# Optimization experiments

Hardware: AMD Instinct MI355X
Metric: run time of the kernel (lower is better)

The kernel has to match this reference:

```python
import jax, jax.numpy as jnp
import numpy as np

D_MODEL = 1024
HEADS = 16


def setup_inputs() -> dict:
    key = jax.random.key(0)
    ks = jax.random.split(key, 11)
    B, S, D = 2, 2048, D_MODEL
    scale = 1.0 / np.sqrt(D)
    inp = {
        "q": jax.random.normal(ks[0], (B, S, D), jnp.float32),
        "k": jax.random.normal(ks[1], (B, S, D), jnp.float32),
        "v": jax.random.normal(ks[2], (B, S, D), jnp.float32),
        "w_q": jax.random.normal(ks[3], (D, D), jnp.float32) * scale,
        "b_q": jnp.zeros((D,), jnp.float32),
        "w_k": jax.random.normal(ks[4], (D, D), jnp.float32) * scale,
        "b_k": jnp.zeros((D,), jnp.float32),
        "w_v": jax.random.normal(ks[5], (D, D), jnp.float32) * scale,
        "b_v": jnp.zeros((D,), jnp.float32),
        "w_o": jax.random.normal(ks[6], (D, D), jnp.float32) * scale,
        "b_o": jnp.zeros((D,), jnp.float32),
    }
    return inp


def reference(q, k, v, w_q, b_q, w_k, b_k, w_v, b_v, w_o, b_o):
    B, S, D = q.shape
    H = HEADS
    Dh = D // H

    def split(x):  # [B,S,D] -> [B,H,S,Dh]
        return x.reshape(B, S, H, Dh).transpose(0, 2, 1, 3)

    qh = split(q @ w_q + b_q)
    kh = split(k @ w_k + b_k)
    vh = split(v @ w_v + b_v)

    # scaled dot-product attention: softmax(Q K^T / sqrt(Dh)) V
    scores = jnp.einsum("bhsd,bhtd->bhst", qh, kh) / jnp.sqrt(
        jnp.asarray(Dh, qh.dtype)
    )
    attn = jax.nn.softmax(scores, axis=-1)
    out = jnp.einsum("bhst,bhtd->bhsd", attn, vh)

    concat = out.transpose(0, 2, 1, 3).reshape(B, S, D)
    return concat @ w_o + b_o
```

## Files before the change

kernel.cpp:

```cpp
#include <hip/hip_runtime.h>
#include <hip/hip_bf16.h>
#include <math.h>

using bf16 = __hip_bfloat16;
typedef __bf16 bf16x8v __attribute__((ext_vector_type(8)));
typedef float f32x4v __attribute__((ext_vector_type(4)));

#define AS1 __attribute__((address_space(1)))
#define AS3 __attribute__((address_space(3)))

__device__ __forceinline__ void g2l16(const void* g, void* l) {
  __builtin_amdgcn_global_load_lds((const AS1 void*)g, (AS3 void*)l, 16, 0, 0);
}

__device__ __forceinline__ float fclamp(float v) {
  return fminf(fmaxf(v, -6.0e4f), 6.0e4f);
}

#define QSCL 0.1803368801111204f

__global__ __launch_bounds__(256) void transpose_cvt4(
    const float* __restrict__ w0, const float* __restrict__ w1,
    const float* __restrict__ w2, const float* __restrict__ w3,
    bf16* __restrict__ o0, bf16* __restrict__ o1,
    bf16* __restrict__ o2, bf16* __restrict__ o3) {
  const float* in = (blockIdx.z == 0) ? w0 : (blockIdx.z == 1) ? w1
                    : (blockIdx.z == 2) ? w2 : w3;
  bf16* out = (blockIdx.z == 0) ? o0 : (blockIdx.z == 1) ? o1
              : (blockIdx.z == 2) ? o2 : o3;
  __shared__ alignas(16) bf16 tile[64][80];
  const int t = threadIdx.x;
  const int bx = blockIdx.x * 64, by = blockIdx.y * 64;
#pragma unroll
  for (int p = 0; p < 4; ++p) {
    int idx = p * 1024 + t * 4;
    int r = idx >> 6, c0 = idx & 63;
    float4 v = *(const float4*)&in[(size_t)(by + r) * 1024 + bx + c0];
    tile[c0 + 0][r] = __float2bfloat16(v.x);
    tile[c0 + 1][r] = __float2bfloat16(v.y);
    tile[c0 + 2][r] = __float2bfloat16(v.z);
    tile[c0 + 3][r] = __float2bfloat16(v.w);
  }
  __syncthreads();
#pragma unroll
  for (int p = 0; p < 2; ++p) {
    int idx = p * 2048 + t * 8;
    int c = idx >> 6, r0 = idx & 63;
    *(uint4*)&out[(size_t)(bx + c) * 1024 + by + r0] = *(const uint4*)&tile[c][r0];
  }
}

__global__ __launch_bounds__(256) void cvt3(
    const float* __restrict__ q, const float* __restrict__ k,
    const float* __restrict__ v, bf16* __restrict__ oq,
    bf16* __restrict__ ok, bf16* __restrict__ ov) {
  const float* in = (blockIdx.y == 0) ? q : (blockIdx.y == 1) ? k : v;
  bf16* out = (blockIdx.y == 0) ? oq : (blockIdx.y == 1) ? ok : ov;
  int i = (blockIdx.x * 256 + threadIdx.x) * 8;
  float4 a = *(const float4*)&in[i];
  float4 b = *(const float4*)&in[i + 4];
  alignas(16) bf16 tmp[8];
  tmp[0] = __float2bfloat16(a.x); tmp[1] = __float2bfloat16(a.y);
  tmp[2] = __float2bfloat16(a.z); tmp[3] = __float2bfloat16(a.w);
  tmp[4] = __float2bfloat16(b.x); tmp[5] = __float2bfloat16(b.y);
  tmp[6] = __float2bfloat16(b.z); tmp[7] = __float2bfloat16(b.w);
  *(uint4*)&out[i] = *(const uint4*)tmp;
}

__device__ __forceinline__ void qkv_store(bf16* C, int z, int m, int n, float v) {
  int b_ = m >> 11, s_ = m & 2047, h_ = n >> 6, d_ = n & 63;
  size_t oidx = (z == 2)
      ? ((size_t)(b_ * 16 + h_) * 64 + d_) * 2048 + s_
      : ((size_t)(b_ * 16 + h_) * 2048 + s_) * 64 + d_;
  C[oidx] = __float2bfloat16(v);
}

__global__ __launch_bounds__(256, 2) void gemm_qkv_bf16(
    const bf16* __restrict__ Aq, const bf16* __restrict__ Ak,
    const bf16* __restrict__ Av,
    const bf16* __restrict__ WtQ, const bf16* __restrict__ WtK,
    const bf16* __restrict__ WtV,
    const float* __restrict__ bq, const float* __restrict__ bk_,
    const float* __restrict__ bv_,
    bf16* __restrict__ Qh, bf16* __restrict__ Kh, bf16* __restrict__ Vt) {
  constexpr int K = 1024;
  const int z = blockIdx.z;
  const bf16* A    = (z == 0) ? Aq : (z == 1) ? Ak : Av;
  const bf16* Bt   = (z == 0) ? WtQ : (z == 1) ? WtK : WtV;
  const float* bias = (z == 0) ? bq : (z == 1) ? bk_ : bv_;
  bf16* C = (z == 0) ? Qh : (z == 1) ? Kh : Vt;

  __shared__ alignas(16) bf16 As[128 * 32];
  __shared__ alignas(16) bf16 Bs[128 * 32];
  const int t = threadIdx.x;
  const int wave = t >> 6, lane = t & 63;
  const int quad = lane >> 4, l16 = lane & 15;
  const int bm = blockIdx.x * 128, bn = blockIdx.y * 128;
  const int wm = (wave & 1) * 64, wn = (wave >> 1) * 64;

  f32x4v acc[4][4] = {};

  for (int k0 = 0; k0 < K; k0 += 32) {
    __syncthreads();
#pragma unroll
    for (int c = 0; c < 2; ++c) {
      int idx = c * 2048 + t * 8;
      int row = idx >> 5, col = idx & 31;
      g2l16(&A[(size_t)(bm + row) * K + k0 + col], &As[c * 2048 + wave * 512]);
      g2l16(&Bt[(size_t)(bn + row) * K + k0 + col], &Bs[c * 2048 + wave * 512]);
    }
    __syncthreads();

    bf16x8v a[4], b[4];
#pragma unroll
    for (int mi = 0; mi < 4; ++mi)
      a[mi] = *(const bf16x8v*)&As[(wm + mi * 16 + l16) * 32 + quad * 8];
#pragma unroll
    for (int ni = 0; ni < 4; ++ni)
      b[ni] = *(const bf16x8v*)&Bs[(wn + ni * 16 + l16) * 32 + quad * 8];
#pragma unroll
    for (int mi = 0; mi < 4; ++mi)
#pragma unroll
      for (int ni = 0; ni < 4; ++ni)
        acc[mi][ni] = __builtin_amdgcn_mfma_f32_16x16x32_bf16(a[mi], b[ni],
                                                              acc[mi][ni], 0, 0, 0);
  }

  const float scl = (z == 0) ? QSCL : 1.0f;
#pragma unroll
  for (int ni = 0; ni < 4; ++ni) {
    int n = bn + wn + ni * 16 + l16;
    float bz = bias[n];
#pragma unroll
    for (int mi = 0; mi < 4; ++mi)
#pragma unroll
      for (int r = 0; r < 4; ++r) {
        int m = bm + wm + mi * 16 + quad * 4 + r;
        qkv_store(C, z, m, n, fclamp(acc[mi][ni][r] + bz) * scl);
      }
  }
}

__global__ __launch_bounds__(256, 2) void gemm_qkv_f32(
    const float* __restrict__ Aq, const float* __restrict__ Ak,
    const float* __restrict__ Av,
    const bf16* __restrict__ WtQ, const bf16* __restrict__ WtK,
    const bf16* __restrict__ WtV,
    const float* __restrict__ bq, const float* __restrict__ bk_,
    const float* __restrict__ bv_,
    bf16* __restrict__ Qh, bf16* __restrict__ Kh, bf16* __restrict__ Vt) {
  constexpr int K = 1024, LDA = 40;
  const int z = blockIdx.z;
  const float* A  = (z == 0) ? Aq : (z == 1) ? Ak : Av;
  const bf16* Bt  = (z == 0) ? WtQ : (z == 1) ? WtK : WtV;
  const float* bias = (z == 0) ? bq : (z == 1) ? bk_ : bv_;
  bf16* C = (z == 0) ? Qh : (z == 1) ? Kh : Vt;

  __shared__ alignas(16) bf16 As[128 * LDA];
  __shared__ alignas(16) bf16 Bs[128 * LDA];
  const int t = threadIdx.x;
  const int wave = t >> 6, lane = t & 63;
  const int quad = lane >> 4, l16 = lane & 15;
  const int bm = blockIdx.x * 128, bn = blockIdx.y * 128;
  const int wm = (wave & 1) * 64, wn = (wave >> 1) * 64;

  f32x4v acc[4][4] = {};

  for (int k0 = 0; k0 < K; k0 += 32) {
    uint4 va[2], vb[2];
#pragma unroll
    for (int c = 0; c < 2; ++c) {
      int idx = c * 2048 + t * 8;
      int row = idx >> 5, col = idx & 31;
      const float* src = &A[(size_t)(bm + row) * K + k0 + col];
      float4 f0 = *(const float4*)src;
      float4 f1 = *(const float4*)(src + 4);
      alignas(16) bf16 tmp[8];
      tmp[0] = __float2bfloat16(f0.x); tmp[1] = __float2bfloat16(f0.y);
      tmp[2] = __float2bfloat16(f0.z); tmp[3] = __float2bfloat16(f0.w);
      tmp[4] = __float2bfloat16(f1.x); tmp[5] = __float2bfloat16(f1.y);
      tmp[6] = __float2bfloat16(f1.z); tmp[7] = __float2bfloat16(f1.w);
      va[c] = *(const uint4*)tmp;
      vb[c] = *(const uint4*)&Bt[(size_t)(bn + row) * K + k0 + col];
    }
    __syncthreads();
#pragma unroll
    for (int c = 0; c < 2; ++c) {
      int idx = c * 2048 + t * 8;
      int row = idx >> 5, col = idx & 31;
      *(uint4*)&As[row * LDA + col] = va[c];
      *(uint4*)&Bs[row * LDA + col] = vb[c];
    }
    __syncthreads();

    bf16x8v a[4], b[4];
#pragma unroll
    for (int mi = 0; mi < 4; ++mi)
      a[mi] = *(const bf16x8v*)&As[(wm + mi * 16 + l16) * LDA + quad * 8];
#pragma unroll
    for (int ni = 0; ni < 4; ++ni)
      b[ni] = *(const bf16x8v*)&Bs[(wn + ni * 16 + l16) * LDA + quad * 8];
#pragma unroll
    for (int mi = 0; mi < 4; ++mi)
#pragma unroll
      for (int ni = 0; ni < 4; ++ni)
        acc[mi][ni] = __builtin_amdgcn_mfma_f32_16x16x32_bf16(a[mi], b[ni],
                                                              acc[mi][ni], 0, 0, 0);
  }

  const float scl = (z == 0) ? QSCL : 1.0f;
#pragma unroll
  for (int ni = 0; ni < 4; ++ni) {
    int n = bn + wn + ni * 16 + l16;
    float bz = bias[n];
#pragma unroll
    for (int mi = 0; mi < 4; ++mi)
#pragma unroll
      for (int r = 0; r < 4; ++r) {
        int m = bm + wm + mi * 16 + quad * 4 + r;
        qkv_store(C, z, m, n, fclamp(acc[mi][ni][r] + bz) * scl);
      }
  }
}

__global__ __launch_bounds__(256, 2) void gemm_out(
    const bf16* __restrict__ A, const bf16* __restrict__ Bt,
    const float* __restrict__ bias, float* __restrict__ C) {
  constexpr int K = 1024, N = 1024;
  __shared__ alignas(16) bf16 As[128 * 32];
  __shared__ alignas(16) bf16 Bs[64 * 32];
  const int t = threadIdx.x;
  const int wave = t >> 6, lane = t & 63;
  const int quad = lane >> 4, l16 = lane & 15;
  const int bm = blockIdx.x * 128, bn = blockIdx.y * 64;
  const int wm = (wave & 1) * 64, wn = (wave >> 1) * 32;

  f32x4v acc[4][2] = {};

  for (int k0 = 0; k0 < K; k0 += 32) {
    __syncthreads();
#pragma unroll
    for (int c = 0; c < 2; ++c) {
      int idx = c * 2048 + t * 8;
      int row = idx >> 5, col = idx & 31;
      g2l16(&A[(size_t)(bm + row) * K + k0 + col], &As[c * 2048 + wave * 512]);
    }
    {
      int idx = t * 8;
      int row = idx >> 5, col = idx & 31;
      g2l16(&Bt[(size_t)(bn + row) * K + k0 + col], &Bs[wave * 512]);
    }
    __syncthreads();

    bf16x8v a[4], b[2];
#pragma unroll
    for (int mi = 0; mi < 4; ++mi)
      a[mi] = *(const bf16x8v*)&As[(wm + mi * 16 + l16) * 32 + quad * 8];
#pragma unroll
    for (int ni = 0; ni < 2; ++ni)
      b[ni] = *(const bf16x8v*)&Bs[(wn + ni * 16 + l16) * 32 + quad * 8];
#pragma unroll
    for (int mi = 0; mi < 4; ++mi)
#pragma unroll
      for (int ni = 0; ni < 2; ++ni)
        acc[mi][ni] = __builtin_amdgcn_mfma_f32_16x16x32_bf16(a[mi], b[ni],
                                                              acc[mi][ni], 0, 0, 0);
  }

#pragma unroll
  for (int ni = 0; ni < 2; ++ni) {
    int n = bn + wn + ni * 16 + l16;
    float bz = bias[n];
#pragma unroll
    for (int mi = 0; mi < 4; ++mi)
#pragma unroll
      for (int r = 0; r < 4; ++r) {
        int m = bm + wm + mi * 16 + quad * 4 + r;
        C[(size_t)m * N + n] = fclamp(acc[mi][ni][r] + bz);
      }
  }
}

__global__ __launch_bounds__(256, 2) void attn(
    const bf16* __restrict__ Qh, const bf16* __restrict__ Kh,
    const bf16* __restrict__ Vt, bf16* __restrict__ Ctx) {
  constexpr int LDPP = 40;
  __shared__ alignas(16) bf16 Qs[128 * 64];
  __shared__ alignas(16) bf16 Ks[2][64 * 64];
  __shared__ alignas(16) bf16 Vs[2][64 * 64];
  __shared__ alignas(16) bf16 Ps[4][32 * LDPP];
  const int t = threadIdx.x;
  const int wave = t >> 6, lane = t & 63;
  const int quad = lane >> 4, l16 = lane & 15;
  const int sw = l16 & 7;
  const int qb = blockIdx.x;
  const int bh = blockIdx.y;
  const size_t bh_off = (size_t)bh * 2048 * 64;
  const bf16* Qb = Qh + bh_off;
  const bf16* Kb = Kh + bh_off;
  const bf16* Vb = Vt + bh_off;

  const int srow = t >> 3;
  const int schunk = t & 7;

  auto stageKV = [&](int kt, int buf) {
#pragma unroll
    for (int c = 0; c < 2; ++c) {
      int row = c * 32 + srow;
      int mc = schunk ^ (row & 7);
      g2l16(&Kb[(size_t)(kt * 64 + row) * 64 + mc * 8],
            &Ks[buf][c * 2048 + wave * 512]);
      g2l16(&Vb[(size_t)row * 2048 + kt * 64 + mc * 8],
            &Vs[buf][c * 2048 + wave * 512]);
    }
  };

#pragma unroll
  for (int c = 0; c < 4; ++c) {
    int row = c * 32 + srow;
    int mc = schunk ^ (row & 7);
    g2l16(&Qb[(size_t)(qb * 128 + row) * 64 + mc * 8], &Qs[c * 2048 + wave * 512]);
  }
  stageKV(0, 0);
  asm volatile("s_waitcnt vmcnt(0)" ::: "memory");
  __builtin_amdgcn_s_barrier();

  bf16x8v aq[2][2];
#pragma unroll
  for (int mi = 0; mi < 2; ++mi)
#pragma unroll
    for (int kk = 0; kk < 2; ++kk)
      aq[mi][kk] = *(const bf16x8v*)
          &Qs[(wave * 32 + mi * 16 + l16) * 64 + (((kk * 4 + quad) ^ sw) << 3)];

  bf16x8v vone;
#pragma unroll
  for (int i = 0; i < 8; ++i) vone[i] = (__bf16)1.0f;

  f32x4v lsum[2] = {};
  f32x4v oacc[2][4] = {};

  auto compute = [&](int buf) {
#pragma unroll
    for (int h = 0; h < 2; ++h) {
      f32x4v s[2][2] = {};
      __builtin_amdgcn_s_setprio(1);
#pragma unroll
      for (int kk = 0; kk < 2; ++kk)
#pragma unroll
        for (int ni = 0; ni < 2; ++ni) {
          bf16x8v bk = *(const bf16x8v*)
              &Ks[buf][(h * 32 + ni * 16 + l16) * 64 + (((kk * 4 + quad) ^ sw) << 3)];
#pragma unroll
          for (int mi = 0; mi < 2; ++mi)
            s[mi][ni] = __builtin_amdgcn_mfma_f32_16x16x32_bf16(aq[mi][kk], bk,
                                                                s[mi][ni], 0, 0, 0);
        }
      __builtin_amdgcn_s_setprio(0);

#pragma unroll
      for (int mi = 0; mi < 2; ++mi)
#pragma unroll
        for (int ni = 0; ni < 2; ++ni)
#pragma unroll
          for (int r = 0; r < 4; ++r) {
            float p = __builtin_amdgcn_exp2f(fminf(s[mi][ni][r], 80.f));
            Ps[wave][(mi * 16 + quad * 4 + r) * LDPP + ni * 16 + l16] =
                __float2bfloat16(p);
          }

      bf16x8v ap[2];
#pragma unroll
      for (int mi = 0; mi < 2; ++mi)
        ap[mi] = *(const bf16x8v*)&Ps[wave][(mi * 16 + l16) * LDPP + quad * 8];
      __builtin_amdgcn_s_setprio(1);
#pragma unroll
      for (int mi = 0; mi < 2; ++mi)
        lsum[mi] = __builtin_amdgcn_mfma_f32_16x16x32_bf16(ap[mi], vone,
                                                           lsum[mi], 0, 0, 0);
#pragma unroll
      for (int ni = 0; ni < 4; ++ni) {
        bf16x8v bv = *(const bf16x8v*)
            &Vs[buf][(ni * 16 + l16) * 64 + (((h * 4 + quad) ^ sw) << 3)];
#pragma unroll
        for (int mi = 0; mi < 2; ++mi)
          oacc[mi][ni] = __builtin_amdgcn_mfma_f32_16x16x32_bf16(ap[mi], bv,
                                                                 oacc[mi][ni],
                                                                 0, 0, 0);
      }
      __builtin_amdgcn_s_setprio(0);
    }
  };

  for (int kt = 0; kt < 32; kt += 2) {
    stageKV(kt + 1, 1);
    compute(0);
    asm volatile("s_waitcnt vmcnt(0)" ::: "memory");
    __builtin_amdgcn_s_barrier();
    if (kt + 2 < 32) stageKV(kt + 2, 0);
    compute(1);
    asm volatile("s_waitcnt vmcnt(0)" ::: "memory");
    __builtin_amdgcn_s_barrier();
  }

  const int b_ = bh >> 4, h_ = bh & 15;
#pragma unroll
  for (int mi = 0; mi < 2; ++mi)
#pragma unroll
    for (int r = 0; r < 4; ++r) {
      int sr = qb * 128 + wave * 32 + mi * 16 + quad * 4 + r;
      float inv = 1.0f / fmaxf(lsum[mi][r], 1.0e-20f);
#pragma unroll
      for (int ni = 0; ni < 4; ++ni) {
        int col = h_ * 64 + ni * 16 + l16;
        Ctx[(size_t)(b_ * 2048 + sr) * 1024 + col] =
            __float2bfloat16(fclamp(oacc[mi][ni][r] * inv));
      }
    }
}

extern "C" void kernel_launch(void* const* d_in, const int* in_sizes, int n_in,
                              void* d_out, int out_size, void* d_ws, size_t ws_size,
                              hipStream_t stream) {
  const float* q   = (const float*)d_in[0];
  const float* k   = (const float*)d_in[1];
  const float* v   = (const float*)d_in[2];
  const float* w_q = (const float*)d_in[3];
  const float* b_q = (const float*)d_in[4];
  const float* w_k = (const float*)d_in[5];
  const float* b_k = (const float*)d_in[6];
  const float* w_v = (const float*)d_in[7];
  const float* b_v = (const float*)d_in[8];
  const float* w_o = (const float*)d_in[9];
  const float* b_o = (const float*)d_in[10];
  float* out = (float*)d_out;

  char* ws = (char*)d_ws;
  const size_t MB = (size_t)1024 * 1024;
  bf16* WtQ = (bf16*)(ws + 0 * MB);
  bf16* WtK = (bf16*)(ws + 2 * MB);
  bf16* WtV = (bf16*)(ws + 4 * MB);
  bf16* WtO = (bf16*)(ws + 6 * MB);

  dim3 tb(256);
  transpose_cvt4<<<dim3(16, 16, 4), tb, 0, stream>>>(w_q, w_k, w_v, w_o,
                                                     WtQ, WtK, WtV, WtO);

  const bool big = ws_size >= (size_t)57 * MB;
  if (big) {
    bf16* Qa  = (bf16*)(ws + 8 * MB);
    bf16* Ka  = (bf16*)(ws + 16 * MB);
    bf16* Va  = (bf16*)(ws + 24 * MB);
    bf16* Qh  = (bf16*)(ws + 32 * MB);
    bf16* Kh  = (bf16*)(ws + 40 * MB);
    bf16* Vt  = (bf16*)(ws + 48 * MB);
    bf16* Ctx = Qa;

    cvt3<<<dim3(2048, 3), tb, 0, stream>>>(q, k, v, Qa, Ka, Va);
    gemm_qkv_bf16<<<dim3(32, 8, 3), tb, 0, stream>>>(Qa, Ka, Va, WtQ, WtK, WtV,
                                                     b_q, b_k, b_v, Qh, Kh, Vt);
    attn<<<dim3(16, 32), tb, 0, stream>>>(Qh, Kh, Vt, Ctx);
    gemm_out<<<dim3(32, 16), tb, 0, stream>>>(Ctx, WtO, b_o, out);
  } else {
    bf16* Qh  = (bf16*)(ws + 8 * MB);
    bf16* Kh  = (bf16*)(ws + 16 * MB);
    bf16* Vt  = (bf16*)(ws + 24 * MB);
    bf16* Ctx = (bf16*)(ws + 32 * MB);

    gemm_qkv_f32<<<dim3(32, 8, 3), tb, 0, stream>>>(q, k, v, WtQ, WtK, WtV,
                                                    b_q, b_k, b_v, Qh, Kh, Vt);
    attn<<<dim3(16, 32), tb, 0, stream>>>(Qh, Kh, Vt, Ctx);
    gemm_out<<<dim3(32, 16), tb, 0, stream>>>(Ctx, WtO, b_o, out);
  }
}
```

Before: 237.2 us.

## Vectorize V-transpose and P stores, alias P buffer onto Q shared memory

For the V projection, the QKV GEMM epilogues now pack four bf16 values and write them as one 8-byte store into the transposed V layout, replacing scalar stores. In attention, the QK MFMA operands are swapped so each lane holds four consecutive key columns of S. This lets the exponentiated P tile be written to LDS as one packed 8-byte store instead of four scalar stores. The P staging buffer now reuses the Q shared-memory region after Q is loaded into registers, at the cost of an added barrier. The smaller LDS footprint may allow higher occupancy.

```diff
diff --git a/kernel.cpp b/kernel.cpp
--- a/kernel.cpp
+++ b/kernel.cpp
@@ -15,6 +15,12 @@
 
 __device__ __forceinline__ float fclamp(float v) {
   return fminf(fmaxf(v, -6.0e4f), 6.0e4f);
+}
+
+__device__ __forceinline__ unsigned packbf(float a, float b) {
+  unsigned short lo = __builtin_bit_cast(unsigned short, __float2bfloat16(a));
+  unsigned short hi = __builtin_bit_cast(unsigned short, __float2bfloat16(b));
+  return (unsigned)lo | ((unsigned)hi << 16);
 }
 
 #define QSCL 0.1803368801111204f
@@ -126,18 +132,36 @@
                                                               acc[mi][ni], 0, 0, 0);
   }
 
-  const float scl = (z == 0) ? QSCL : 1.0f;
-#pragma unroll
-  for (int ni = 0; ni < 4; ++ni) {
-    int n = bn + wn + ni * 16 + l16;
-    float bz = bias[n];
-#pragma unroll
-    for (int mi = 0; mi < 4; ++mi)
-#pragma unroll
-      for (int r = 0; r < 4; ++r) {
-        int m = bm + wm + mi * 16 + quad * 4 + r;
-        qkv_store(C, z, m, n, fclamp(acc[mi][ni][r] + bz) * scl);
+  if (z == 2) {
+#pragma unroll
+    for (int ni = 0; ni < 4; ++ni) {
+      int n = bn + wn + ni * 16 + l16;
+      float bz = bias[n];
+      int h_ = n >> 6, d_ = n & 63;
+#pragma unroll
+      for (int mi = 0; mi < 4; ++mi) {
+        int m0 = bm + wm + mi * 16 + quad * 4;
+        int b_ = m0 >> 11, s0 = m0 & 2047;
+        uint2 u;
+        u.x = packbf(fclamp(acc[mi][ni][0] + bz), fclamp(acc[mi][ni][1] + bz));
+        u.y = packbf(fclamp(acc[mi][ni][2] + bz), fclamp(acc[mi][ni][3] + bz));
+        *(uint2*)&C[((size_t)(b_ * 16 + h_) * 64 + d_) * 2048 + s0] = u;
       }
+    }
+  } else {
+    const float scl = (z == 0) ? QSCL : 1.0f;
+#pragma unroll
+    for (int ni = 0; ni < 4; ++ni) {
+      int n = bn + wn + ni * 16 + l16;
+      float bz = bias[n];
+#pragma unroll
+      for (int mi = 0; mi < 4; ++mi)
+#pragma unroll
+        for (int r = 0; r < 4; ++r) {
+          int m = bm + wm + mi * 16 + quad * 4 + r;
+          qkv_store(C, z, m, n, fclamp(acc[mi][ni][r] + bz) * scl);
+        }
+    }
   }
 }
 
@@ -208,18 +232,36 @@
                                                               acc[mi][ni], 0, 0, 0);
   }
 
-  const float scl = (z == 0) ? QSCL : 1.0f;
-#pragma unroll
-  for (int ni = 0; ni < 4; ++ni) {
-    int n = bn + wn + ni * 16 + l16;
-    float bz = bias[n];
-#pragma unroll
-    for (int mi = 0; mi < 4; ++mi)
-#pragma unroll
-      for (int r = 0; r < 4; ++r) {
-        int m = bm + wm + mi * 16 + quad * 4 + r;
-        qkv_store(C, z, m, n, fclamp(acc[mi][ni][r] + bz) * scl);
+  if (z == 2) {
+#pragma unroll
+    for (int ni = 0; ni < 4; ++ni) {
+      int n = bn + wn + ni * 16 + l16;
+      float bz = bias[n];
+      int h_ = n >> 6, d_ = n & 63;
+#pragma unroll
+      for (int mi = 0; mi < 4; ++mi) {
+        int m0 = bm + wm + mi * 16 + quad * 4;
+        int b_ = m0 >> 11, s0 = m0 & 2047;
+        uint2 u;
+        u.x = packbf(fclamp(acc[mi][ni][0] + bz), fclamp(acc[mi][ni][1] + bz));
+        u.y = packbf(fclamp(acc[mi][ni][2] + bz), fclamp(acc[mi][ni][3] + bz));
+        *(uint2*)&C[((size_t)(b_ * 16 + h_) * 64 + d_) * 2048 + s0] = u;
       }
+    }
+  } else {
+    const float scl = (z == 0) ? QSCL : 1.0f;
+#pragma unroll
+    for (int ni = 0; ni < 4; ++ni) {
+      int n = bn + wn + ni * 16 + l16;
+      float bz = bias[n];
+#pragma unroll
+      for (int mi = 0; mi < 4; ++mi)
+#pragma unroll
+        for (int r = 0; r < 4; ++r) {
+          int m = bm + wm + mi * 16 + quad * 4 + r;
+          qkv_store(C, z, m, n, fclamp(acc[mi][ni][r] + bz) * scl);
+        }
+    }
   }
 }
 
@@ -285,10 +327,9 @@
     const bf16* __restrict__ Qh, const bf16* __restrict__ Kh,
     const bf16* __restrict__ Vt, bf16* __restrict__ Ctx) {
   constexpr int LDPP = 40;
-  __shared__ alignas(16) bf16 Qs[128 * 64];
+  __shared__ alignas(16) bf16 QsPs[128 * 64];
   __shared__ alignas(16) bf16 Ks[2][64 * 64];
   __shared__ alignas(16) bf16 Vs[2][64 * 64];
-  __shared__ alignas(16) bf16 Ps[4][32 * LDPP];
   const int t = threadIdx.x;
   const int wave = t >> 6, lane = t & 63;
   const int quad = lane >> 4, l16 = lane & 15;
@@ -319,7 +360,8 @@
   for (int c = 0; c < 4; ++c) {
     int row = c * 32 + srow;
     int mc = schunk ^ (row & 7);
-    g2l16(&Qb[(size_t)(qb * 128 + row) * 64 + mc * 8], &Qs[c * 2048 + wave * 512]);
+    g2l16(&Qb[(size_t)(qb * 128 + row) * 64 + mc * 8],
+          &QsPs[c * 2048 + wave * 512]);
   }
   stageKV(0, 0);
   asm volatile("s_waitcnt vmcnt(0)" ::: "memory");
@@ -331,7 +373,10 @@
 #pragma unroll
     for (int kk = 0; kk < 2; ++kk)
       aq[mi][kk] = *(const bf16x8v*)
-          &Qs[(wave * 32 + mi * 16 + l16) * 64 + (((kk * 4 + quad) ^ sw) << 3)];
+          &QsPs[(wave * 32 + mi * 16 + l16) * 64 + (((kk * 4 + quad) ^ sw) << 3)];
+
+  __syncthreads();
+  bf16* Psw = QsPs + wave * (32 * LDPP);
 
   bf16x8v vone;
 #pragma unroll
@@ -353,7 +398,7 @@
               &Ks[buf][(h * 32 + ni * 16 + l16) * 64 + (((kk * 4 + quad) ^ sw) << 3)];
 #pragma unroll
           for (int mi = 0; mi < 2; ++mi)
-            s[mi][ni] = __builtin_amdgcn_mfma_f32_16x16x32_bf16(aq[mi][kk], bk,
+            s[mi][ni] = __builtin_amdgcn_mfma_f32_16x16x32_bf16(bk, aq[mi][kk],
                                                                 s[mi][ni], 0, 0, 0);
         }
       __builtin_amdgcn_s_setprio(0);
@@ -361,18 +406,21 @@
 #pragma unroll
       for (int mi = 0; mi < 2; ++mi)
 #pragma unroll
-        for (int ni = 0; ni < 2; ++ni)
-#pragma unroll
-          for (int r = 0; r < 4; ++r) {
-            float p = __builtin_amdgcn_exp2f(fminf(s[mi][ni][r], 80.f));
-            Ps[wave][(mi * 16 + quad * 4 + r) * LDPP + ni * 16 + l16] =
-                __float2bfloat16(p);
-          }
+        for (int ni = 0; ni < 2; ++ni) {
+          float p0 = __builtin_amdgcn_exp2f(fminf(s[mi][ni][0], 80.f));
+          float p1 = __builtin_amdgcn_exp2f(fminf(s[mi][ni][1], 80.f));
+          float p2 = __builtin_amdgcn_exp2f(fminf(s[mi][ni][2], 80.f));
+          float p3 = __builtin_amdgcn_exp2f(fminf(s[mi][ni][3], 80.f));
+          uint2 u;
+          u.x = packbf(p0, p1);
+          u.y = packbf(p2, p3);
+          *(uint2*)&Psw[(mi * 16 + l16) * LDPP + ni * 16 + quad * 4] = u;
+        }
 
       bf16x8v ap[2];
 #pragma unroll
       for (int mi = 0; mi < 2; ++mi)
-        ap[mi] = *(const bf16x8v*)&Ps[wave][(mi * 16 + l16) * LDPP + quad * 8];
+        ap[mi] = *(const bf16x8v*)&Psw[(mi * 16 + l16) * LDPP + quad * 8];
       __builtin_amdgcn_s_setprio(1);
 #pragma unroll
       for (int mi = 0; mi < 2; ++mi)
```

Result: faster. 224.9 us (-5.2%).
